# Optimization experiments

Hardware: AMD Instinct MI355X
Metric: run time of the kernel (lower is better)

Reference implementation:

```python
import jax, jax.numpy as jnp
import numpy as np
import math

B, C, H, W = 8, 256, 64, 64
G = 32           # norm_groups
IMG_C = 3        # image_channels * wavelet_components
EPS = 1e-5


def group_norm(x, gamma, beta):
    # x: [B, C, H, W]; normalize over (C//G, H, W) within each of G groups
    b, c, h, w = x.shape
    xg = x.reshape(b, G, c // G, h, w)
    mean = xg.mean(axis=(2, 3, 4), keepdims=True)
    var = xg.var(axis=(2, 3, 4), keepdims=True)
    xg = (xg - mean) * jax.lax.rsqrt(var + EPS)
    x = xg.reshape(b, c, h, w)
    return x * gamma[None, :, None, None] + beta[None, :, None, None]


def conv1x1(x, weight):
    # weight: [out_c, in_c]; 1x1 conv == channel matmul
    return jnp.einsum('oc,bchw->bohw', weight, x)


def setup_inputs() -> dict:
    key = jax.random.key(0)
    ks = jax.random.split(key, 8)
    s_q = 1.0 / math.sqrt(IMG_C)
    s_kv = 1.0 / math.sqrt(C)
    return {
        'input': jax.random.normal(ks[0], (B, C, H, W), jnp.float32),
        'quary': jax.random.normal(ks[1], (B, IMG_C, H, W), jnp.float32),
        'gn_weight': jnp.ones((C,), jnp.float32),
        'gn_bias': jnp.zeros((C,), jnp.float32),
        'w_q': jax.random.uniform(ks[2], (C, IMG_C), jnp.float32, -s_q, s_q),
        'w_kv': jax.random.uniform(ks[3], (2 * C, C), jnp.float32, -s_kv, s_kv),
        'w_out': jax.random.uniform(ks[4], (C, C), jnp.float32, -s_kv, s_kv),
        'b_out': jax.random.uniform(ks[5], (C,), jnp.float32, -s_kv, s_kv),
    }


def reference(input, quary, gn_weight, gn_bias, w_q, w_kv, w_out, b_out):
    b, c, h, w = input.shape
    norm = group_norm(input, gn_weight, gn_bias)
    kv = conv1x1(norm, w_kv)                      # [B, 2C, H, W]
    key_t, value = kv[:, :c], kv[:, c:]           # each [B, C, H, W]
    q = conv1x1(quary, w_q)                       # [B, C, H, W]
    # attention over all spatial positions, single head, head_dim = C
    attn = jnp.einsum('bchw,bcyx->bhwyx', q, key_t) / math.sqrt(c)
    attn = jax.nn.softmax(attn.reshape(b, h, w, h * w), axis=-1)
    attn = attn.reshape(b, h, w, h, w)
    out = jnp.einsum('bhwyx,bcyx->bchw', attn, value)  # [B, C, H, W]
    out = conv1x1(out, w_out) + b_out[None, :, None, None]
    return out + input
```

## Files before the change

### kernel.cpp

```cpp
#include <hip/hip_runtime.h>

typedef unsigned short u16;
typedef unsigned int   u32;
typedef float  f32x4  __attribute__((ext_vector_type(4)));
typedef float  fltx4  __attribute__((ext_vector_type(4)));
typedef float  f32x2  __attribute__((ext_vector_type(2)));
typedef short  bf16x8 __attribute__((ext_vector_type(8)));
typedef u32    u32x4  __attribute__((ext_vector_type(4)));
typedef u32    u32x2  __attribute__((ext_vector_type(2)));

#define CDIM 256
#define NPIX 4096
#define QSCALE 0.09016843736f

__device__ __forceinline__ u16 f2bf(float f) {
  u32 u = __builtin_bit_cast(u32, f);
  u += 0x7fffu + ((u >> 16) & 1u);
  return (u16)(u >> 16);
}
__device__ __forceinline__ float bf2f(u16 h) {
  return __builtin_bit_cast(float, (u32)h << 16);
}

#if __has_builtin(__builtin_amdgcn_exp2f)
#define FEXP2 __builtin_amdgcn_exp2f
#else
#define FEXP2 exp2f
#endif

#define LO2(v) __builtin_shufflevector(v, v, 0, 1)
#define HI2(v) __builtin_shufflevector(v, v, 2, 3)

union U8 { bf16x8 v; u16 u[8]; u32 w[4]; };

__device__ __forceinline__ void llds16(u16* lds_base, const u16* gsrc) {
  __builtin_amdgcn_global_load_lds(
      (const __attribute__((address_space(1))) unsigned int*)gsrc,
      (__attribute__((address_space(3))) unsigned int*)lds_base, 16, 0, 0);
}

__global__ __launch_bounds__(1024) void gn_stats_prep(
    const float* __restrict__ x, const float* __restrict__ wkv,
    const float* __restrict__ wout, const float* __restrict__ wq,
    float* __restrict__ stats, u16* __restrict__ w16, float* __restrict__ wq3p) {
  const int bid = blockIdx.x, tid = threadIdx.x;
  if (bid < 256) {
    const float* base = x + (long)bid * 32768;
    float s = 0.f, s2 = 0.f;
    for (int i = tid; i < 8192; i += 1024) {
      fltx4 v = ((const fltx4*)base)[i];
      s  += v[0] + v[1] + v[2] + v[3];
      s2 += v[0]*v[0] + v[1]*v[1] + v[2]*v[2] + v[3]*v[3];
    }
    for (int off = 1; off < 64; off <<= 1) {
      s  += __shfl_xor(s, off);
      s2 += __shfl_xor(s2, off);
    }
    __shared__ float red[32];
    int w = tid >> 6;
    if ((tid & 63) == 0) { red[w] = s; red[16 + w] = s2; }
    __syncthreads();
    if (tid < 16) {
      s  = red[tid];
      s2 = red[16 + tid];
      for (int off = 1; off < 16; off <<= 1) {
        s  += __shfl_xor(s, off);
        s2 += __shfl_xor(s2, off);
      }
      if (tid == 0) {
        float mean = s * (1.f / 32768.f);
        float var  = s2 * (1.f / 32768.f) - mean * mean;
        stats[bid * 2]     = mean;
        stats[bid * 2 + 1] = rsqrtf(var + 1e-5f);
      }
    }
    return;
  }
  const int blk = bid - 256;
  if (blk < 4) {
    const float* s = (blk < 2 ? wkv + 65536 : wout) + (blk & 1) * 32768;
    u16* d = w16 + (blk >> 1) * 65536 + (blk & 1) * 32768;
    for (int i = tid * 4; i < 32768; i += 4096) {
      fltx4 v = *(const fltx4*)(s + i);
      u32x2 o;
      o[0] = (u32)f2bf(v[0]) | ((u32)f2bf(v[1]) << 16);
      o[1] = (u32)f2bf(v[2]) | ((u32)f2bf(v[3]) << 16);
      *(u32x2*)(d + i) = o;
    }
  } else if (tid < 256) {
    const int p = blk - 4, c = tid;
    float a0 = 0.f, a1 = 0.f, a2 = 0.f;
    for (int o = p * 64; o < p * 64 + 64; ++o) {
      float kv = wkv[o * 256 + c];
      a0 += wq[o * 3 + 0] * kv;
      a1 += wq[o * 3 + 1] * kv;
      a2 += wq[o * 3 + 2] * kv;
    }
    float* dst = wq3p + (p * 256 + c) * 4;
    dst[0] = a0 * QSCALE; dst[1] = a1 * QSCALE; dst[2] = a2 * QSCALE; dst[3] = 0.f;
  }
}

#define TSTR 264
__global__ __launch_bounds__(256) void gn_fused(const float* __restrict__ x,
                                                const float* __restrict__ stats,
                                                const float* __restrict__ gamma,
                                                const float* __restrict__ beta,
                                                const float* __restrict__ wq3p,
                                                const u16* __restrict__ w16v,
                                                u16* __restrict__ Vv,
                                                float* __restrict__ K3x,
                                                float* __restrict__ K3y,
                                                float* __restrict__ K3z) {
  __shared__ u16 tile[64 * TSTR];
  __shared__ float wl4[256 * 4];
  __shared__ float part[4][64][4];
  const int tid = threadIdx.x;
  const int b = blockIdx.y, nb = blockIdx.x * 64;
  const int nIn = tid & 63, c4 = tid >> 6;
  const int lane = tid & 63;
  const int m = lane & 15, quad = lane >> 4;
  {
    const f32x4* wp = (const f32x4*)wq3p;
    *(f32x4*)&wl4[tid * 4] = wp[tid] + wp[256 + tid] + wp[512 + tid] + wp[768 + tid];
  }
  const float* xb = x + (long)b * (CDIM * NPIX);
  #pragma unroll
  for (int p8 = 0; p8 < 8; ++p8) {
    U8 pk;
    #pragma unroll
    for (int e = 0; e < 8; ++e) {
      int c = c4 * 64 + p8 * 8 + e;
      int g = c >> 3;
      float mean = stats[(b * 32 + g) * 2];
      float rstd = stats[(b * 32 + g) * 2 + 1];
      float v = xb[(long)c * NPIX + nb + nIn];
      pk.u[e] = f2bf((v - mean) * rstd * gamma[c] + beta[c]);
    }
    *(bf16x8*)&tile[nIn * TSTR + c4 * 64 + p8 * 8] = pk.v;
  }
  __syncthreads();
  {
    float a0 = 0.f, a1 = 0.f, a2 = 0.f;
    #pragma unroll
    for (int p8 = 0; p8 < 8; ++p8) {
      U8 v; v.v = *(const bf16x8*)&tile[nIn * TSTR + c4 * 64 + p8 * 8];
      #pragma unroll
      for (int e = 0; e < 8; ++e) {
        int c = c4 * 64 + p8 * 8 + e;
        float f = bf2f(v.u[e]);
        const f32x4 wv = *(const f32x4*)&wl4[c * 4];
        a0 += f * wv[0]; a1 += f * wv[1]; a2 += f * wv[2];
      }
    }
    part[c4][nIn][0] = a0; part[c4][nIn][1] = a1; part[c4][nIn][2] = a2;
  }
  __syncthreads();
  if (c4 == 0) {
    float s0 = part[0][nIn][0] + part[1][nIn][0] + part[2][nIn][0] + part[3][nIn][0];
    float s1 = part[0][nIn][1] + part[1][nIn][1] + part[2][nIn][1] + part[3][nIn][1];
    float s2 = part[0][nIn][2] + part[1][nIn][2] + part[2][nIn][2] + part[3][nIn][2];
    long idx = (long)b * NPIX + nb + nIn;
    K3x[idx] = s0; K3y[idx] = s1; K3z[idx] = s2;
  }
  f32x4 acc[4][4] = {};
  #pragma unroll
  for (int ks = 0; ks < 8; ++ks) {
    const int kb = ks * 32;
    bf16x8 av[4], bv[4];
    #pragma unroll
    for (int i = 0; i < 4; ++i)
      av[i] = *(const bf16x8*)&w16v[(c4 * 64 + i * 16 + m) * 256 + kb + quad * 8];
    #pragma unroll
    for (int i = 0; i < 4; ++i)
      bv[i] = *(const bf16x8*)&tile[(i * 16 + m) * TSTR + kb + quad * 8];
    #pragma unroll
    for (int mi = 0; mi < 4; ++mi)
      #pragma unroll
      for (int ni = 0; ni < 4; ++ni)
        acc[mi][ni] = __builtin_amdgcn_mfma_f32_16x16x32_bf16(av[mi], bv[ni], acc[mi][ni], 0, 0, 0);
  }
  u16* Vb = Vv + (long)b * (CDIM * NPIX);
  #pragma unroll
  for (int mi = 0; mi < 4; ++mi)
    #pragma unroll
    for (int r = 0; r < 4; ++r) {
      int o = c4 * 64 + mi * 16 + quad * 4 + r;
      #pragma unroll
      for (int ni = 0; ni < 4; ++ni)
        Vb[(long)o * NPIX + nb + ni * 16 + m] = f2bf(acc[mi][ni][r]);
    }
}

__global__ __launch_bounds__(256, 4) void gemm_out(
    const u16* __restrict__ Ap, const u16* __restrict__ B0,
    const u16* __restrict__ B1, const float* __restrict__ ls,
    float* __restrict__ out, const float* __restrict__ bias,
    const float* __restrict__ resid) {
  __shared__ u16 Als[64 * 72];
  __shared__ u16 Bls[128 * 72];
  __shared__ float invB[128];
  const int tid = threadIdx.x;
  const int lane = tid & 63;
  const int m = lane & 15, quad = lane >> 4;
  const int wid = tid >> 6;
  const int wm = wid & 1, wn = wid >> 1;
  const int m0 = blockIdx.x * 64, n0 = blockIdx.y * 128;
  const int bz = blockIdx.z;
  const long S = (long)NPIX * CDIM;

  if (tid < 128) {
    long n = (long)bz * 4096 + n0 + tid;
    invB[tid] = 1.f / (ls[n] + ls[32768 + n]);
  }
  __syncthreads();

  f32x4 acc[2][4] = {};

  for (int ks = 0; ks < 4; ++ks) {
    const int kb = ks * 64;
    if (ks) __syncthreads();
    #pragma unroll
    for (int it = 0; it < 2; ++it) {
      int idx = it * 2048 + tid * 8;
      int r = idx >> 6, c = idx & 63;
      *(u32x4*)&Als[r * 72 + c] = *(const u32x4*)(Ap + (long)(m0 + r) * CDIM + kb + c);
    }
    {
      const u16* s0 = B0 + S * bz;
      const u16* s1 = B1 + S * bz;
      #pragma unroll
      for (int it = 0; it < 4; ++it) {
        int idx = it * 2048 + tid * 8;
        int r = idx >> 6, c = idx & 63;
        long off = (long)(n0 + r) * CDIM + kb + c;
        u32x4 A0 = *(const u32x4*)(s0 + off);
        u32x4 A1 = *(const u32x4*)(s1 + off);
        float inv = invB[r];
        u32x4 o;
        #pragma unroll
        for (int i = 0; i < 4; ++i) {
          float lo = (bf2f((u16)(A0[i] & 0xffff)) + bf2f((u16)(A1[i] & 0xffff))) * inv;
          float hi = (bf2f((u16)(A0[i] >> 16))    + bf2f((u16)(A1[i] >> 16)))    * inv;
          o[i] = (u32)f2bf(lo) | ((u32)f2bf(hi) << 16);
        }
        *(u32x4*)&Bls[r * 72 + c] = o;
      }
    }
    __syncthreads();
    #pragma unroll
    for (int s = 0; s < 2; ++s) {
      bf16x8 av[2], bv[4];
      #pragma unroll
      for (int i = 0; i < 2; ++i)
        av[i] = *(const bf16x8*)&Als[(wm * 32 + i * 16 + m) * 72 + s * 32 + quad * 8];
      #pragma unroll
      for (int i = 0; i < 4; ++i)
        bv[i] = *(const bf16x8*)&Bls[(wn * 64 + i * 16 + m) * 72 + s * 32 + quad * 8];
      #pragma unroll
      for (int mi = 0; mi < 2; ++mi)
        #pragma unroll
        for (int ni = 0; ni < 4; ++ni)
          acc[mi][ni] = __builtin_amdgcn_mfma_f32_16x16x32_bf16(av[mi], bv[ni], acc[mi][ni], 0, 0, 0);
    }
  }

  const int row0 = m0 + wm * 32;
  const int col0 = n0 + wn * 64 + m;
  float* ob = out + S * bz;
  const float* res = resid + S * bz;
  #pragma unroll
  for (int mi = 0; mi < 2; ++mi)
    #pragma unroll
    for (int r = 0; r < 4; ++r) {
      int row = row0 + mi * 16 + quad * 4 + r;
      float bs = bias[row];
      #pragma unroll
      for (int ni = 0; ni < 4; ++ni) {
        long off = (long)row * NPIX + col0 + ni * 16;
        ob[off] = acc[mi][ni][r] + bs + res[off];
      }
    }
}

#define MFMA16(a, bfr, c) __builtin_amdgcn_mfma_f32_16x16x32_bf16(a, bfr, c, 0, 0, 0)

#define P_LOAD(ks, JB)                                                      \
  {                                                                         \
    const int jo_ = (JB) + (ks) * 32 + quad * 8;                            \
    kx0 = *(const fltx4*)(Kx + jo_); kx1 = *(const fltx4*)(Kx + jo_ + 4);   \
    ky0 = *(const fltx4*)(Ky + jo_); ky1 = *(const fltx4*)(Ky + jo_ + 4);   \
    kz0 = *(const fltx4*)(Kz + jo_); kz1 = *(const fltx4*)(Kz + jo_ + 4);   \
  }

#define P_EXP(PB, ks)                                                       \
  {                                                                         \
    f32x2 xc_[4] = {LO2(kx0), HI2(kx0), LO2(kx1), HI2(kx1)};                \
    f32x2 yc_[4] = {LO2(ky0), HI2(ky0), LO2(ky1), HI2(ky1)};                \
    f32x2 zc_[4] = {LO2(kz0), HI2(kz0), LO2(kz1), HI2(kz1)};                \
    _Pragma("unroll")                                                       \
    for (int qm_ = 0; qm_ < 2; ++qm_) {                                     \
      _Pragma("unroll")                                                     \
      for (int c2_ = 0; c2_ < 4; ++c2_) {                                   \
        f32x2 s_ = xc_[c2_] * y2[qm_][0] + yc_[c2_] * y2[qm_][1]            \
                 + zc_[c2_] * y2[qm_][2];                                   \
        float p0_ = FEXP2(s_[0]);                                           \
        float p1_ = FEXP2(s_[1]);                                           \
        u32 r0_ = __builtin_bit_cast(u32, p0_) + 0x8000u;                   \
        u32 r1_ = __builtin_bit_cast(u32, p1_) + 0x8000u;                   \
        PB[qm_][ks].w[c2_] = (r0_ >> 16) | (r1_ & 0xffff0000u);             \
        f32x2 pv_; pv_[0] = p0_; pv_[1] = p1_;                              \
        lsv[qm_] += pv_;                                                    \
      }                                                                     \
    }                                                                       \
  }

#define PV_GROUP(PB, CT0)                                                   \
  _Pragma("unroll")                                                         \
  for (int ct_ = (CT0); ct_ < (CT0) + 4; ++ct_) {                           \
    int c_ = ct_ * 16 + m;                                                  \
    bf16x8 a0_ = *(const bf16x8*)&Vb[c_ * 64 + (((quad)     ^ (c_ & 7)) << 3)]; \
    bf16x8 a1_ = *(const bf16x8*)&Vb[c_ * 64 + (((4 + quad) ^ (c_ & 7)) << 3)]; \
    acc[0][ct_] = MFMA16(a0_, PB[0][0].v, acc[0][ct_]);                     \
    acc[1][ct_] = MFMA16(a0_, PB[1][0].v, acc[1][ct_]);                     \
    acc[0][ct_] = MFMA16(a1_, PB[0][1].v, acc[0][ct_]);                     \
    acc[1][ct_] = MFMA16(a1_, PB[1][1].v, acc[1][ct_]);                     \
  }

__global__ __launch_bounds__(256, 2) void attn_kernel(
    const float* __restrict__ quary,
    const float* __restrict__ K3x, const float* __restrict__ K3y,
    const float* __restrict__ K3z,
    const u16* __restrict__ V, u16* __restrict__ Op0, u16* __restrict__ Op1,
    float* __restrict__ lsum) {
  __shared__ u16 VLS[2][256 * 64];
  const int lane = threadIdx.x & 63, w = threadIdx.x >> 6;
  const int m = lane & 15, quad = lane >> 4;
  const int b = blockIdx.z, half = blockIdx.y;
  const int qb = blockIdx.x * 128 + w * 32;

  f32x2 y2[2][3];
  #pragma unroll
  for (int qm = 0; qm < 2; ++qm) {
    int n = qb + qm * 16 + m;
    float q0 = quary[b * 12288 + n];
    float q1 = quary[b * 12288 + 4096 + n];
    float q2 = quary[b * 12288 + 8192 + n];
    y2[qm][0][0] = q0; y2[qm][0][1] = q0;
    y2[qm][1][0] = q1; y2[qm][1][1] = q1;
    y2[qm][2][0] = q2; y2[qm][2][1] = q2;
  }

  const float* Kx = K3x + (long)b * NPIX + half * 2048;
  const float* Ky = K3y + (long)b * NPIX + half * 2048;
  const float* Kz = K3z + (long)b * NPIX + half * 2048;
  const u16* VG = V + (long)b * CDIM * NPIX + half * 2048;

  int srcV[8];
  #pragma unroll
  for (int i = 0; i < 8; ++i) {
    int c = (w * 8 + i) * 8 + (lane >> 3);
    srcV[i] = c * NPIX + (((lane & 7) ^ (c & 7)) << 3);
  }

  f32x2 lsv[2] = {};
  f32x4 acc[2][16] = {};
  U8 pbA[2][2], pbB[2][2];
  fltx4 kx0, kx1, ky0, ky1, kz0, kz1;

  #pragma unroll
  for (int i = 0; i < 8; ++i)
    llds16(VLS[0] + (w * 8 + i) * 512, VG + srcV[i]);

  P_LOAD(0, 0); P_EXP(pbA, 0);
  P_LOAD(1, 0); P_EXP(pbA, 1);

  for (int kt = 0; kt < 31; ++kt) {
    __syncthreads();
    #pragma unroll
    for (int i = 0; i < 8; ++i)
      llds16(VLS[(kt + 1) & 1] + (w * 8 + i) * 512, VG + srcV[i] + (kt + 1) * 64);
    const u16* Vb = VLS[kt & 1];
    const int JB = (kt + 1) * 64;

    P_LOAD(0, JB);
    __builtin_amdgcn_s_setprio(1);
    PV_GROUP(pbA, 0);
    PV_GROUP(pbA, 4);
    __builtin_amdgcn_s_setprio(0);
    P_EXP(pbB, 0);
    P_LOAD(1, JB);
    __builtin_amdgcn_s_setprio(1);
    PV_GROUP(pbA, 8);
    PV_GROUP(pbA, 12);
    __builtin_amdgcn_s_setprio(0);
    P_EXP(pbB, 1);

    pbA[0][0] = pbB[0][0]; pbA[0][1] = pbB[0][1];
    pbA[1][0] = pbB[1][0]; pbA[1][1] = pbB[1][1];
  }
  {
    __syncthreads();
    const u16* Vb = VLS[1];
    __builtin_amdgcn_s_setprio(1);
    PV_GROUP(pbA, 0);
    PV_GROUP(pbA, 4);
    PV_GROUP(pbA, 8);
    PV_GROUP(pbA, 12);
    __builtin_amdgcn_s_setprio(0);
  }

  u16* OpB = (half ? Op1 : Op0);
  #pragma unroll
  for (int qm = 0; qm < 2; ++qm) {
    int n = qb + qm * 16 + m;
    u16* row = OpB + ((long)b * NPIX + n) * CDIM + quad * 4;
    #pragma unroll
    for (int ct = 0; ct < 16; ++ct) {
      u32x2 o;
      o[0] = (u32)f2bf(acc[qm][ct][0]) | ((u32)f2bf(acc[qm][ct][1]) << 16);
      o[1] = (u32)f2bf(acc[qm][ct][2]) | ((u32)f2bf(acc[qm][ct][3]) << 16);
      *(u32x2*)(row + ct * 16) = o;
    }
    float ls = lsv[qm][0] + lsv[qm][1];
    ls += __shfl_xor(ls, 16);
    ls += __shfl_xor(ls, 32);
    if (lane < 16)
      lsum[(long)half * 32768 + (long)b * NPIX + n] = ls;
  }
}

extern "C" void kernel_launch(void* const* d_in, const int* in_sizes, int n_in,
                              void* d_out, int out_size, void* d_ws, size_t ws_size,
                              hipStream_t stream) {
  (void)in_sizes; (void)n_in; (void)out_size; (void)ws_size;
  const float* input = (const float*)d_in[0];
  const float* quary = (const float*)d_in[1];
  const float* gnw   = (const float*)d_in[2];
  const float* gnb   = (const float*)d_in[3];
  const float* wq    = (const float*)d_in[4];
  const float* wkv   = (const float*)d_in[5];
  const float* wout  = (const float*)d_in[6];
  const float* bout  = (const float*)d_in[7];
  float* out = (float*)d_out;

  char* ws = (char*)d_ws;
  float* stats = (float*)ws;
  float* wq3p  = (float*)(ws + 4096);
  float* lsum  = (float*)(ws + 20480);
  float* K3x   = (float*)(ws + 282624);
  float* K3y   = (float*)(ws + 413696);
  float* K3z   = (float*)(ws + 544768);
  u16* w16   = (u16*)(ws + 675840);
  const long base = 937984;
  u16* Vv    = (u16*)(ws + base);
  u16* Op0   = (u16*)(ws + base + 1L * 16777216);
  u16* Op1   = (u16*)(ws + base + 2L * 16777216);

  gn_stats_prep<<<264, 1024, 0, stream>>>(input, wkv, wout, wq, stats, w16, wq3p);
  gn_fused<<<dim3(64, 8), 256, 0, stream>>>(input, stats, gnw, gnb, wq3p,
                                            w16, Vv, K3x, K3y, K3z);
  attn_kernel<<<dim3(32, 2, 8), 256, 0, stream>>>(quary, K3x, K3y, K3z, Vv, Op0, Op1, lsum);
  gemm_out<<<dim3(4, 32, 8), 256, 0, stream>>>(
      w16 + 65536, Op0, Op1, lsum, out, bout, input);
}
```

Baseline: 235.9 us.

## Fold split-attention merge into GEMM K loop and use direct LDS loads

```diff
diff --git a/kernel.cpp b/kernel.cpp
--- a/kernel.cpp
+++ b/kernel.cpp
@@ -197,14 +197,14 @@
     const u16* __restrict__ B1, const float* __restrict__ ls,
     float* __restrict__ out, const float* __restrict__ bias,
     const float* __restrict__ resid) {
-  __shared__ u16 Als[64 * 72];
-  __shared__ u16 Bls[128 * 72];
+  __shared__ u16 Als[64 * 64];
+  __shared__ u16 Bls[128 * 64];
   __shared__ float invB[128];
   const int tid = threadIdx.x;
   const int lane = tid & 63;
+  const int w = tid >> 6;
   const int m = lane & 15, quad = lane >> 4;
-  const int wid = tid >> 6;
-  const int wm = wid & 1, wn = wid >> 1;
+  const int wm = w & 1, wn = w >> 1;
   const int m0 = blockIdx.x * 64, n0 = blockIdx.y * 128;
   const int bz = blockIdx.z;
   const long S = (long)NPIX * CDIM;
@@ -215,48 +215,43 @@
   }
   __syncthreads();
 
+  const int slotOff = ((lane & 7) ^ (lane >> 3)) * 8;
+  int srcA[2], srcB[4];
+  #pragma unroll
+  for (int it = 0; it < 2; ++it) {
+    int row = (w * 2 + it) * 8 + (lane >> 3);
+    srcA[it] = (m0 + row) * CDIM + slotOff;
+  }
+  #pragma unroll
+  for (int it = 0; it < 4; ++it) {
+    int row = (w * 4 + it) * 8 + (lane >> 3);
+    srcB[it] = (n0 + row) * CDIM + slotOff;
+  }
+
   f32x4 acc[2][4] = {};
 
-  for (int ks = 0; ks < 4; ++ks) {
-    const int kb = ks * 64;
+  #pragma unroll
+  for (int ks = 0; ks < 8; ++ks) {
+    const int kb = (ks & 3) * 64;
+    const u16* Bsrc = (ks < 4 ? B0 : B1) + S * bz;
     if (ks) __syncthreads();
     #pragma unroll
-    for (int it = 0; it < 2; ++it) {
-      int idx = it * 2048 + tid * 8;
-      int r = idx >> 6, c = idx & 63;
-      *(u32x4*)&Als[r * 72 + c] = *(const u32x4*)(Ap + (long)(m0 + r) * CDIM + kb + c);
-    }
-    {
-      const u16* s0 = B0 + S * bz;
-      const u16* s1 = B1 + S * bz;
-      #pragma unroll
-      for (int it = 0; it < 4; ++it) {
-        int idx = it * 2048 + tid * 8;
-        int r = idx >> 6, c = idx & 63;
-        long off = (long)(n0 + r) * CDIM + kb + c;
-        u32x4 A0 = *(const u32x4*)(s0 + off);
-        u32x4 A1 = *(const u32x4*)(s1 + off);
-        float inv = invB[r];
-        u32x4 o;
-        #pragma unroll
-        for (int i = 0; i < 4; ++i) {
-          float lo = (bf2f((u16)(A0[i] & 0xffff)) + bf2f((u16)(A1[i] & 0xffff))) * inv;
-          float hi = (bf2f((u16)(A0[i] >> 16))    + bf2f((u16)(A1[i] >> 16)))    * inv;
-          o[i] = (u32)f2bf(lo) | ((u32)f2bf(hi) << 16);
-        }
-        *(u32x4*)&Bls[r * 72 + c] = o;
-      }
-    }
+    for (int it = 0; it < 2; ++it)
+      llds16(Als + (w * 2 + it) * 512, Ap + srcA[it] + kb);
+    #pragma unroll
+    for (int it = 0; it < 4; ++it)
+      llds16(Bls + (w * 4 + it) * 512, Bsrc + (long)srcB[it] + kb);
     __syncthreads();
     #pragma unroll
     for (int s = 0; s < 2; ++s) {
+      const int chunk = ((s * 4 + quad) ^ (m & 7)) * 8;
       bf16x8 av[2], bv[4];
       #pragma unroll
       for (int i = 0; i < 2; ++i)
-        av[i] = *(const bf16x8*)&Als[(wm * 32 + i * 16 + m) * 72 + s * 32 + quad * 8];
+        av[i] = *(const bf16x8*)&Als[(wm * 32 + i * 16 + m) * 64 + chunk];
       #pragma unroll
       for (int i = 0; i < 4; ++i)
-        bv[i] = *(const bf16x8*)&Bls[(wn * 64 + i * 16 + m) * 72 + s * 32 + quad * 8];
+        bv[i] = *(const bf16x8*)&Bls[(wn * 64 + i * 16 + m) * 64 + chunk];
       #pragma unroll
       for (int mi = 0; mi < 2; ++mi)
         #pragma unroll
@@ -269,6 +264,10 @@
   const int col0 = n0 + wn * 64 + m;
   float* ob = out + S * bz;
   const float* res = resid + S * bz;
+  float iv[4];
+  #pragma unroll
+  for (int ni = 0; ni < 4; ++ni)
+    iv[ni] = invB[wn * 64 + ni * 16 + m];
   #pragma unroll
   for (int mi = 0; mi < 2; ++mi)
     #pragma unroll
@@ -278,7 +277,7 @@
       #pragma unroll
       for (int ni = 0; ni < 4; ++ni) {
         long off = (long)row * NPIX + col0 + ni * 16;
-        ob[off] = acc[mi][ni][r] + bs + res[off];
+        ob[off] = acc[mi][ni][r] * iv[ni] + bs + res[off];
       }
     }
 }
@@ -384,16 +383,12 @@
     const int JB = (kt + 1) * 64;
 
     P_LOAD(0, JB);
-    __builtin_amdgcn_s_setprio(1);
     PV_GROUP(pbA, 0);
     PV_GROUP(pbA, 4);
-    __builtin_amdgcn_s_setprio(0);
     P_EXP(pbB, 0);
     P_LOAD(1, JB);
-    __builtin_amdgcn_s_setprio(1);
     PV_GROUP(pbA, 8);
     PV_GROUP(pbA, 12);
-    __builtin_amdgcn_s_setprio(0);
     P_EXP(pbB, 1);
 
     pbA[0][0] = pbB[0][0]; pbA[0][1] = pbB[0][1];
@@ -402,12 +397,10 @@
   {
     __syncthreads();
     const u16* Vb = VLS[1];
-    __builtin_amdgcn_s_setprio(1);
     PV_GROUP(pbA, 0);
     PV_GROUP(pbA, 4);
     PV_GROUP(pbA, 8);
     PV_GROUP(pbA, 12);
-    __builtin_amdgcn_s_setprio(0);
   }
 
   u16* OpB = (half ? Op1 : Op0);
```

Result: faster. 231.2 us (-2.0%).
